# Kernel tuning notes

Measured on AMD Instinct MI355X. Metric: run time of the kernel, lower is better.

## Reference

```python
import jax, jax.numpy as jnp
import numpy as np

MUL = 128          # shared multiplicity 'u' appended to all operands
DIM_IN = 4         # SO3 '0+1' -> 1 + 3 components
DIM_OUT = 4        # SO3 '0+1'
BATCH = 32768
NPATH = (2, 5, 12)  # coupling paths ('w' dim) for degree 1,2,3
BLOCK_ID = np.array([0, 1, 1, 1])  # irrep block of each of the 4 components


def setup_inputs() -> dict:
    key = jax.random.key(0)
    ks = jax.random.split(key, 8)
    x = jax.random.normal(ks[0], (BATCH, DIM_IN * MUL), jnp.float32)
    # one (mul,mul) channel-mixing matrix per irrep block, per degree (3 Linears)
    lin_w = jax.random.normal(ks[1], (3, 2, MUL, MUL), jnp.float32)
    # per-degree path weights, shape (num_paths, mul)
    w1 = jax.random.normal(ks[2], (NPATH[0], MUL), jnp.float32)
    w2 = jax.random.normal(ks[3], (NPATH[1], MUL), jnp.float32)
    w3 = jax.random.normal(ks[4], (NPATH[2], MUL), jnp.float32)
    # basis (Clebsch-Gordan-like) coefficient tensors C[a1..av, i, w], normalized
    C1 = jax.random.normal(ks[5], (DIM_IN, DIM_OUT, NPATH[0]), jnp.float32) / np.sqrt(DIM_IN * NPATH[0])
    C2 = jax.random.normal(ks[6], (DIM_IN, DIM_IN, DIM_OUT, NPATH[1]), jnp.float32) / np.sqrt(DIM_IN**2 * NPATH[1])
    C3 = jax.random.normal(ks[7], (DIM_IN, DIM_IN, DIM_IN, DIM_OUT, NPATH[2]), jnp.float32) / np.sqrt(DIM_IN**3 * NPATH[2])
    return {"x": x, "lin_w": lin_w, "w1": w1, "w2": w2, "w3": w3,
            "C1": C1, "C2": C2, "C3": C3}


def _linear(x3, w_deg):
    # x3: (n, dim, u); w_deg: (n_blocks=2, u, u). Per-irrep channel mixing.
    Wd = w_deg[BLOCK_ID]  # (dim, u, u) gathered per component
    return jnp.einsum('ndu,duv->ndv', x3, Wd) / np.sqrt(MUL)


def reference(x, lin_w, w1, w2, w3, C1, C2, C3):
    n = x.shape[0]
    x3 = x.reshape(n, DIM_IN, MUL)  # ir_mul layout: (component, channel)
    y1 = _linear(x3, lin_w[0])
    y2 = _linear(x3, lin_w[1])
    y3 = _linear(x3, lin_w[2])

    # degree 1: out += sum_{a,w} C1[a,i,w] w1[w,u] y1[n,a,u]
    C1u = jnp.einsum('aiw,wu->aiu', C1, w1)
    out = jnp.einsum('aiu,nau->niu', C1u, y1)

    # degree 2
    C2u = jnp.einsum('abiw,wu->abiu', C2, w2)
    T2 = jnp.einsum('abiu,nau->nbiu', C2u, y1)
    out = out + jnp.einsum('nbiu,nbu->niu', T2, y2)

    # degree 3 (staged to keep intermediates at (n, d, d, u) / (n, d, i, u))
    C3u = jnp.einsum('abciw,wu->abciu', C3, w3)
    G = jnp.einsum('nau,nbu->nabu', y1, y2)
    H = jnp.einsum('abciu,nabu->nciu', C3u, G)
    out = out + jnp.einsum('nciu,ncu->niu', H, y3)

    return out.reshape(n, DIM_OUT * MUL)
```

## Files before the change

### kernel.cpp

```cpp
#include <hip/hip_runtime.h>

typedef __attribute__((ext_vector_type(4))) float    f32x4;
typedef __attribute__((ext_vector_type(4))) short    s16x4;
typedef __attribute__((ext_vector_type(8))) short    s16x8;
typedef __attribute__((ext_vector_type(8))) _Float16 h16x8;

#define ROWS 16
#define XS_STRIDE 520
#define NTILE 8

__device__ __forceinline__ short f2bf(float f) {
  unsigned u = __float_as_uint(f);
  u = (u + 0x7fffu + ((u >> 16) & 1u)) >> 16;
  return (short)u;
}

__global__ void precompute_kernel(const float* __restrict__ lin_w,
                                  const float* __restrict__ w1,
                                  const float* __restrict__ w2,
                                  const float* __restrict__ w3,
                                  const float* __restrict__ C1,
                                  const float* __restrict__ C2,
                                  const float* __restrict__ C3,
                                  short*    __restrict__ wF,
                                  _Float16* __restrict__ cc,
                                  float*    __restrict__ cu1) {
  int tid = blockIdx.x * blockDim.x + threadIdx.x;
  int nth = gridDim.x * blockDim.x;
  const float rs = 0.088388347648318447f;
  for (int idx = tid; idx < 6 * 8 * 4 * 64 * 8; idx += nth) {
    int j  = idx & 7;
    int ln = (idx >> 3) & 63;
    int kt = (idx >> 9) & 3;
    int vt = (idx >> 11) & 7;
    int d2 = idx >> 14;
    int v  = vt * 16 + (ln & 15);
    int k  = kt * 32 + (ln >> 4) * 8 + j;
    wF[idx] = f2bf(lin_w[(d2 * 128 + k) * 128 + v] * rs);
  }
  for (int idx = tid; idx < 128 * 16 * 20; idx += nth) {
    int v  = idx / 320;
    int r  = idx - v * 320;
    int ab = r / 20;
    int j  = r - ab * 20;
    int a = ab >> 2, b = ab & 3;
    float s = 0.f;
    if (j < 16) {
      int c = j >> 2, i = j & 3;
      const float* p = C3 + (((a * 4 + b) * 4 + c) * 4 + i) * 12;
      #pragma unroll
      for (int w = 0; w < 12; ++w) s += p[w] * w3[w * 128 + v];
    } else {
      int i = j - 16;
      const float* p = C2 + ((a * 4 + b) * 4 + i) * 5;
      #pragma unroll
      for (int w = 0; w < 5; ++w) s += p[w] * w2[w * 128 + v];
    }
    int byte_in_row = (ab * 48 + j * 2) ^ ((v & 7) << 4);
    cc[v * 384 + (byte_in_row >> 1)] = (_Float16)s;
  }
  for (int idx = tid; idx < 128 * 16; idx += nth) {
    int v = idx >> 4;
    int ai = idx & 15;
    int a = ai >> 2, i = ai & 3;
    cu1[idx] = C1[(a * 4 + i) * 2 + 0] * w1[v] + C1[(a * 4 + i) * 2 + 1] * w1[128 + v];
  }
}

__launch_bounds__(512, 2)
__global__ void main_kernel(const float* __restrict__ x,
                            const short* __restrict__ wF,
                            const _Float16* __restrict__ cc,
                            const float* __restrict__ cu1,
                            float* __restrict__ out) {
  __shared__ short xs[2][ROWS * XS_STRIDE];
  __shared__ __align__(16) char ccl[98304];

  const int t    = threadIdx.x;
  const int lane = t & 63;
  const int wave = t >> 6;
  const int vl   = lane & 15;
  const int quad = lane >> 4;
  const int b    = blockIdx.x;
  const int v    = wave * 16 + vl;

  s16x8 wreg[6][4];
  #pragma unroll
  for (int d2 = 0; d2 < 6; ++d2) {
    const s16x8* wsrc = (const s16x8*)wF + (d2 * 8 + wave) * 256 + lane;
    #pragma unroll
    for (int kt = 0; kt < 4; ++kt) wreg[d2][kt] = wsrc[kt * 64];
  }
  f32x4 c1v[4];
  {
    const f32x4* cu1v = (const f32x4*)(cu1 + v * 16);
    #pragma unroll
    for (int q = 0; q < 4; ++q) c1v[q] = cu1v[q];
  }
  {
    const f32x4* csrc = (const f32x4*)cc;
    f32x4*       cdst = (f32x4*)ccl;
    #pragma unroll
    for (int i = 0; i < 12; ++i) cdst[i * 512 + t] = csrc[i * 512 + t];
  }
  {
    const float4* xsrc = (const float4*)(x + (size_t)b * ROWS * 512);
    #pragma unroll
    for (int i2 = 0; i2 < 4; ++i2) {
      int f = i2 * 512 + t;
      float4 xv = xsrc[f];
      int row = f >> 7, c4 = f & 127;
      s16x4 pk;
      pk[0] = f2bf(xv.x); pk[1] = f2bf(xv.y); pk[2] = f2bf(xv.z); pk[3] = f2bf(xv.w);
      *(s16x4*)&xs[0][row * XS_STRIDE + c4 * 4] = pk;
    }
  }
  __syncthreads();

  float4 xp[4];
  #pragma unroll 1
  for (int k = 0; k < NTILE; ++k) {
    const int cur = k & 1;
    const int n0  = (k * 256 + b) * ROWS;

    if (k + 1 < NTILE) {
      const float4* xsrc = (const float4*)(x + (size_t)((k + 1) * 256 + b) * ROWS * 512);
      #pragma unroll
      for (int i2 = 0; i2 < 4; ++i2) xp[i2] = xsrc[i2 * 512 + t];
    }
    __builtin_amdgcn_sched_barrier(0);

    float yreg[12][4];
    #pragma unroll
    for (int d2 = 0; d2 < 6; ++d2) {
      const int d = d2 >> 1, blk = d2 & 1;
      const int a_begin = blk ? 1 : 0;
      const int a_end   = blk ? 4 : 1;
      #pragma unroll
      for (int a = a_begin; a < a_end; ++a) {
        f32x4 acc4 = {0.f, 0.f, 0.f, 0.f};
        #pragma unroll
        for (int kt = 0; kt < 4; ++kt) {
          s16x8 af = *(const s16x8*)&xs[cur][vl * XS_STRIDE + a * 128 + kt * 32 + quad * 8];
          acc4 = __builtin_amdgcn_mfma_f32_16x16x32_bf16(af, wreg[d2][kt], acc4, 0, 0, 0);
        }
        const int da = d * 4 + a;
        #pragma unroll
        for (int r = 0; r < 4; ++r) yreg[da][r] = acc4[r];
      }
    }

    float acc[4][4];
    {
      float c1[16];
      #pragma unroll
      for (int q = 0; q < 4; ++q) {
        c1[4 * q + 0] = c1v[q][0]; c1[4 * q + 1] = c1v[q][1];
        c1[4 * q + 2] = c1v[q][2]; c1[4 * q + 3] = c1v[q][3];
      }
      #pragma unroll
      for (int i = 0; i < 4; ++i)
        #pragma unroll
        for (int r = 0; r < 4; ++r) {
          float s = c1[0 * 4 + i] * yreg[0][r];
          s = fmaf(c1[1 * 4 + i], yreg[1][r], s);
          s = fmaf(c1[2 * 4 + i], yreg[2][r], s);
          s = fmaf(c1[3 * 4 + i], yreg[3][r], s);
          acc[i][r] = s;
        }
    }

    const char* myc = ccl + v * 768;
    const int   vm  = (v & 7) << 4;
    #pragma unroll
    for (int ab = 0; ab < 16; ++ab) {
      h16x8 h0 = *(const h16x8*)(myc + ((ab * 48 +  0) ^ vm));
      h16x8 h1 = *(const h16x8*)(myc + ((ab * 48 + 16) ^ vm));
      h16x8 h2 = *(const h16x8*)(myc + ((ab * 48 + 32) ^ vm));
      const int a = ab >> 2, b2 = ab & 3;
      float cj[20];
      #pragma unroll
      for (int j = 0; j < 8; ++j) { cj[j] = (float)h0[j]; cj[8 + j] = (float)h1[j]; }
      #pragma unroll
      for (int j = 0; j < 4; ++j) cj[16 + j] = (float)h2[j];
      #pragma unroll
      for (int r = 0; r < 4; ++r) {
        const float G = yreg[a][r] * yreg[4 + b2][r];
        #pragma unroll
        for (int i = 0; i < 4; ++i) {
          float s = cj[16 + i];
          s = fmaf(cj[0 + i],  yreg[8][r],  s);
          s = fmaf(cj[4 + i],  yreg[9][r],  s);
          s = fmaf(cj[8 + i],  yreg[10][r], s);
          s = fmaf(cj[12 + i], yreg[11][r], s);
          acc[i][r] = fmaf(G, s, acc[i][r]);
        }
      }
    }

    #pragma unroll
    for (int r = 0; r < 4; ++r) {
      const int n = n0 + quad * 4 + r;
      #pragma unroll
      for (int i = 0; i < 4; ++i) out[(size_t)n * 512 + i * 128 + v] = acc[i][r];
    }

    if (k + 1 < NTILE) {
      #pragma unroll
      for (int i2 = 0; i2 < 4; ++i2) {
        int f = i2 * 512 + t;
        int row = f >> 7, c4 = f & 127;
        s16x4 pk;
        pk[0] = f2bf(xp[i2].x); pk[1] = f2bf(xp[i2].y);
        pk[2] = f2bf(xp[i2].z); pk[3] = f2bf(xp[i2].w);
        *(s16x4*)&xs[1 - cur][row * XS_STRIDE + c4 * 4] = pk;
      }
    }
    __syncthreads();
  }
}

extern "C" void kernel_launch(void* const* d_in, const int* in_sizes, int n_in,
                              void* d_out, int out_size, void* d_ws, size_t ws_size,
                              hipStream_t stream) {
  const float* x     = (const float*)d_in[0];
  const float* lin_w = (const float*)d_in[1];
  const float* w1    = (const float*)d_in[2];
  const float* w2    = (const float*)d_in[3];
  const float* w3    = (const float*)d_in[4];
  const float* C1    = (const float*)d_in[5];
  const float* C2    = (const float*)d_in[6];
  const float* C3    = (const float*)d_in[7];

  char* ws = (char*)d_ws;
  short*    wF  = (short*)ws;
  _Float16* cc  = (_Float16*)(ws + 196608);
  float*    cu1 = (float*)(ws + 294912);
  float*    out = (float*)d_out;

  hipLaunchKernelGGL(precompute_kernel, dim3(384), dim3(256), 0, stream,
                     lin_w, w1, w2, w3, C1, C2, C3, wF, cc, cu1);
  hipLaunchKernelGGL(main_kernel, dim3(256), dim3(512), 0, stream,
                     x, wF, cc, cu1, out);
}
```

Before: 168.2 us.

## Use 1024-thread blocks with single x buffer and reload weights per iteration

Blocks grow to 1024 threads, with two row-groups of waves covering 32 rows per iteration, and the loop runs 4 times instead of 8. The x tile drops from double buffering to a single LDS buffer, refilled after a barrier once the MFMA stage is done. Linear weights are no longer held in registers for the whole kernel but reloaded from global memory (cache) per degree, and cu1 coefficients move into LDS. The goal is to cut register pressure so 1024-thread blocks fit and more waves hide latency. The cost is repeated weight loads, extra barriers, and less overlap between the x prefetch and compute.

Measured after the change: 530.1 us. 215% more time.

```diff
diff --git a/kernel.cpp b/kernel.cpp
--- a/kernel.cpp
+++ b/kernel.cpp
@@ -5,9 +5,9 @@
 typedef __attribute__((ext_vector_type(8))) short    s16x8;
 typedef __attribute__((ext_vector_type(8))) _Float16 h16x8;
 
-#define ROWS 16
 #define XS_STRIDE 520
-#define NTILE 8
+#define ROWS_BLK 32
+#define NITER 4
 
 __device__ __forceinline__ short f2bf(float f) {
   unsigned u = __float_as_uint(f);
@@ -67,72 +67,61 @@
   }
 }
 
-__launch_bounds__(512, 2)
+__launch_bounds__(1024, 4)
 __global__ void main_kernel(const float* __restrict__ x,
                             const short* __restrict__ wF,
                             const _Float16* __restrict__ cc,
                             const float* __restrict__ cu1,
                             float* __restrict__ out) {
-  __shared__ short xs[2][ROWS * XS_STRIDE];
-  __shared__ __align__(16) char ccl[98304];
+  __shared__ short xs[ROWS_BLK * XS_STRIDE];
+  __shared__ __align__(16) char  ccl[98304];
+  __shared__ __align__(16) float cul[2048];
 
   const int t    = threadIdx.x;
   const int lane = t & 63;
   const int wave = t >> 6;
+  const int rt   = wave >> 3;
+  const int vt   = wave & 7;
   const int vl   = lane & 15;
   const int quad = lane >> 4;
   const int b    = blockIdx.x;
-  const int v    = wave * 16 + vl;
-
-  s16x8 wreg[6][4];
-  #pragma unroll
-  for (int d2 = 0; d2 < 6; ++d2) {
-    const s16x8* wsrc = (const s16x8*)wF + (d2 * 8 + wave) * 256 + lane;
-    #pragma unroll
-    for (int kt = 0; kt < 4; ++kt) wreg[d2][kt] = wsrc[kt * 64];
-  }
-  f32x4 c1v[4];
-  {
-    const f32x4* cu1v = (const f32x4*)(cu1 + v * 16);
-    #pragma unroll
-    for (int q = 0; q < 4; ++q) c1v[q] = cu1v[q];
-  }
+  const int v    = vt * 16 + vl;
+
   {
     const f32x4* csrc = (const f32x4*)cc;
     f32x4*       cdst = (f32x4*)ccl;
     #pragma unroll
-    for (int i = 0; i < 12; ++i) cdst[i * 512 + t] = csrc[i * 512 + t];
-  }
+    for (int i = 0; i < 6; ++i) cdst[i * 1024 + t] = csrc[i * 1024 + t];
+  }
+  if (t < 512) ((f32x4*)cul)[t] = ((const f32x4*)cu1)[t];
   {
-    const float4* xsrc = (const float4*)(x + (size_t)b * ROWS * 512);
+    const float4* xsrc = (const float4*)(x + (size_t)b * ROWS_BLK * 512);
     #pragma unroll
     for (int i2 = 0; i2 < 4; ++i2) {
-      int f = i2 * 512 + t;
+      int f = i2 * 1024 + t;
       float4 xv = xsrc[f];
       int row = f >> 7, c4 = f & 127;
       s16x4 pk;
       pk[0] = f2bf(xv.x); pk[1] = f2bf(xv.y); pk[2] = f2bf(xv.z); pk[3] = f2bf(xv.w);
-      *(s16x4*)&xs[0][row * XS_STRIDE + c4 * 4] = pk;
+      *(s16x4*)&xs[row * XS_STRIDE + c4 * 4] = pk;
     }
   }
   __syncthreads();
 
-  float4 xp[4];
+  float4 xq[4];
   #pragma unroll 1
-  for (int k = 0; k < NTILE; ++k) {
-    const int cur = k & 1;
-    const int n0  = (k * 256 + b) * ROWS;
-
-    if (k + 1 < NTILE) {
-      const float4* xsrc = (const float4*)(x + (size_t)((k + 1) * 256 + b) * ROWS * 512);
-      #pragma unroll
-      for (int i2 = 0; i2 < 4; ++i2) xp[i2] = xsrc[i2 * 512 + t];
-    }
-    __builtin_amdgcn_sched_barrier(0);
+  for (int k = 0; k < NITER; ++k) {
+    const int n0 = (k * 256 + b) * ROWS_BLK + rt * 16;
 
     float yreg[12][4];
     #pragma unroll
     for (int d2 = 0; d2 < 6; ++d2) {
+      s16x8 bf[4];
+      {
+        const s16x8* wsrc = (const s16x8*)wF + (d2 * 8 + vt) * 256 + lane;
+        #pragma unroll
+        for (int kt = 0; kt < 4; ++kt) bf[kt] = wsrc[kt * 64];
+      }
       const int d = d2 >> 1, blk = d2 & 1;
       const int a_begin = blk ? 1 : 0;
       const int a_end   = blk ? 4 : 1;
@@ -141,8 +130,8 @@
         f32x4 acc4 = {0.f, 0.f, 0.f, 0.f};
         #pragma unroll
         for (int kt = 0; kt < 4; ++kt) {
-          s16x8 af = *(const s16x8*)&xs[cur][vl * XS_STRIDE + a * 128 + kt * 32 + quad * 8];
-          acc4 = __builtin_amdgcn_mfma_f32_16x16x32_bf16(af, wreg[d2][kt], acc4, 0, 0, 0);
+          s16x8 af = *(const s16x8*)&xs[(rt * 16 + vl) * XS_STRIDE + a * 128 + kt * 32 + quad * 8];
+          acc4 = __builtin_amdgcn_mfma_f32_16x16x32_bf16(af, bf[kt], acc4, 0, 0, 0);
         }
         const int da = d * 4 + a;
         #pragma unroll
@@ -150,13 +139,24 @@
       }
     }
 
+    __syncthreads();
+
+    if (k + 1 < NITER) {
+      const float4* xsrc = (const float4*)(x + (size_t)((k + 1) * 256 + b) * ROWS_BLK * 512);
+      #pragma unroll
+      for (int i2 = 0; i2 < 4; ++i2) xq[i2] = xsrc[i2 * 1024 + t];
+    }
+    __builtin_amdgcn_sched_barrier(0);
+
     float acc[4][4];
     {
+      const f32x4* c1p = (const f32x4*)(cul + v * 16);
       float c1[16];
       #pragma unroll
       for (int q = 0; q < 4; ++q) {
-        c1[4 * q + 0] = c1v[q][0]; c1[4 * q + 1] = c1v[q][1];
-        c1[4 * q + 2] = c1v[q][2]; c1[4 * q + 3] = c1v[q][3];
+        f32x4 tv = c1p[q];
+        c1[4 * q + 0] = tv[0]; c1[4 * q + 1] = tv[1];
+        c1[4 * q + 2] = tv[2]; c1[4 * q + 3] = tv[3];
       }
       #pragma unroll
       for (int i = 0; i < 4; ++i)
@@ -198,25 +198,25 @@
       }
     }
 
+    if (k + 1 < NITER) {
+      #pragma unroll
+      for (int i2 = 0; i2 < 4; ++i2) {
+        int f = i2 * 1024 + t;
+        int row = f >> 7, c4 = f & 127;
+        s16x4 pk;
+        pk[0] = f2bf(xq[i2].x); pk[1] = f2bf(xq[i2].y);
+        pk[2] = f2bf(xq[i2].z); pk[3] = f2bf(xq[i2].w);
+        *(s16x4*)&xs[row * XS_STRIDE + c4 * 4] = pk;
+      }
+      __syncthreads();
+    }
+
     #pragma unroll
     for (int r = 0; r < 4; ++r) {
       const int n = n0 + quad * 4 + r;
       #pragma unroll
       for (int i = 0; i < 4; ++i) out[(size_t)n * 512 + i * 128 + v] = acc[i][r];
     }
-
-    if (k + 1 < NTILE) {
-      #pragma unroll
-      for (int i2 = 0; i2 < 4; ++i2) {
-        int f = i2 * 512 + t;
-        int row = f >> 7, c4 = f & 127;
-        s16x4 pk;
-        pk[0] = f2bf(xp[i2].x); pk[1] = f2bf(xp[i2].y);
-        pk[2] = f2bf(xp[i2].z); pk[3] = f2bf(xp[i2].w);
-        *(s16x4*)&xs[1 - cur][row * XS_STRIDE + c4 * 4] = pk;
-      }
-    }
-    __syncthreads();
   }
 }
 
@@ -240,6 +240,6 @@
 
   hipLaunchKernelGGL(precompute_kernel, dim3(384), dim3(256), 0, stream,
                      lin_w, w1, w2, w3, C1, C2, C3, wF, cc, cu1);
-  hipLaunchKernelGGL(main_kernel, dim3(256), dim3(512), 0, stream,
+  hipLaunchKernelGGL(main_kernel, dim3(256), dim3(1024), 0, stream,
                      x, wF, cc, cu1, out);
 }
```
